# Kernel optimization log

Measured on AMD Instinct MI355X. Metric: run time of the kernel, lower is better.

Reference implementation:

```python
import jax, jax.numpy as jnp
import numpy as np

B, S, D, H, FF = 2, 2048, 1024, 16, 4096
HD = D // H
EPS = 1e-9


def setup_inputs() -> dict:
    key = jax.random.key(0)
    ks = jax.random.split(key, 16)
    sc = 0.02
    inp = {
        "x": jax.random.normal(ks[0], (B, S, D), jnp.float32),
        "y": jax.random.normal(ks[1], (B, S, D), jnp.float32),
        "decoder_mask": jnp.tril(jnp.ones((S, S), jnp.int32))[None, None],  # [1,1,S,S]
        # self-attention params (weights stored [in,out])
        "qkv_w": jax.random.normal(ks[2], (D, 3 * D), jnp.float32) * sc,
        "qkv_b": jnp.zeros((3 * D,), jnp.float32),
        "sa_fc_w": jax.random.normal(ks[3], (D, D), jnp.float32) * sc,
        "sa_fc_b": jnp.zeros((D,), jnp.float32),
        "g1": jnp.ones((D,), jnp.float32),
        "b1": jnp.zeros((D,), jnp.float32),
        # cross-attention params
        "kv_w": jax.random.normal(ks[4], (D, 2 * D), jnp.float32) * sc,
        "kv_b": jnp.zeros((2 * D,), jnp.float32),
        "q_w": jax.random.normal(ks[5], (D, D), jnp.float32) * sc,
        "q_b": jnp.zeros((D,), jnp.float32),
        "ca_fc_w": jax.random.normal(ks[6], (D, D), jnp.float32) * sc,
        "ca_fc_b": jnp.zeros((D,), jnp.float32),
        "g2": jnp.ones((D,), jnp.float32),
        "b2": jnp.zeros((D,), jnp.float32),
        # FFN params
        "ff1_w": jax.random.normal(ks[7], (D, FF), jnp.float32) * sc,
        "ff1_b": jnp.zeros((FF,), jnp.float32),
        "ff2_w": jax.random.normal(ks[8], (FF, D), jnp.float32) * sc,
        "ff2_b": jnp.zeros((D,), jnp.float32),
        "g3": jnp.ones((D,), jnp.float32),
        "b3": jnp.zeros((D,), jnp.float32),
    }
    return inp


def _layernorm(x, g, b):
    mean = jnp.mean(x, axis=-1, keepdims=True)
    var = jnp.mean((x - mean) ** 2, axis=-1, keepdims=True)
    return g * (x - mean) / jnp.sqrt(var + EPS) + b


def _sdpa(q, k, v, mask=None):
    # q,k,v: [B,H,S,hd]
    scores = jnp.einsum("bhqd,bhkd->bhqk", q, k) / jnp.sqrt(jnp.float32(q.shape[-1]))
    if mask is not None:
        scores = jnp.where(mask == 0, jnp.float32(-1e9), scores)
    attn = jax.nn.softmax(scores, axis=-1)
    return jnp.einsum("bhqk,bhkd->bhqd", attn, v)


def reference(x, y, decoder_mask, qkv_w, qkv_b, sa_fc_w, sa_fc_b, g1, b1,
              kv_w, kv_b, q_w, q_b, ca_fc_w, ca_fc_b, g2, b2,
              ff1_w, ff1_b, ff2_w, ff2_b, g3, b3):
    b, s, d = y.shape
    # --- masked self-attention on y ---
    qkv = (y @ qkv_w + qkv_b).reshape(b, s, H, 3 * HD).transpose(0, 2, 1, 3)
    q, k, v = jnp.split(qkv, 3, axis=-1)
    vals = _sdpa(q, k, v, decoder_mask).transpose(0, 2, 1, 3).reshape(b, s, d)
    sa = vals @ sa_fc_w + sa_fc_b
    y = _layernorm(sa + y, g1, b1)
    # --- cross-attention: kv from x, q from y ---
    kv = (x @ kv_w + kv_b).reshape(b, s, H, 2 * HD).transpose(0, 2, 1, 3)
    k2, v2 = jnp.split(kv, 2, axis=-1)
    q2 = (y @ q_w + q_b).reshape(b, s, H, HD).transpose(0, 2, 1, 3)
    vals2 = _sdpa(q2, k2, v2, None).transpose(0, 2, 1, 3).reshape(b, s, d)
    ca = vals2 @ ca_fc_w + ca_fc_b
    y = _layernorm(ca + y, g2, b2)
    # --- FFN ---
    h = jax.nn.relu(y @ ff1_w + ff1_b)
    ff = h @ ff2_w + ff2_b
    y = _layernorm(ff + y, g3, b3)
    return y
```

## Files before the change

### kernel.cpp

```cpp
#include <hip/hip_runtime.h>

typedef unsigned short u16;
typedef unsigned int u32;
typedef __attribute__((ext_vector_type(4))) float f32x4;
typedef __attribute__((ext_vector_type(8))) __bf16 bf16x8;
typedef __attribute__((ext_vector_type(2))) __bf16 bf16x2;
typedef __attribute__((ext_vector_type(4))) u16 u16x4;

#define NB 2
#define NS 2048
#define ND 1024
#define NH 16
#define NHD 64
#define NFF 4096
#define NBS (NB * NS)

typedef const __attribute__((address_space(1))) unsigned int as1_u32;
typedef __attribute__((address_space(3))) unsigned int as3_u32;

__device__ __forceinline__ void gl_lds16(const u16* g, u16* l) {
  __builtin_amdgcn_global_load_lds((as1_u32*)g, (as3_u32*)l, 16, 0, 0);
}

__device__ __forceinline__ u16 f2bf(float f) {
  union { float f; unsigned u; } v; v.f = f;
  unsigned r = (v.u + 0x7FFFu + ((v.u >> 16) & 1u)) >> 16;
  return (u16)r;
}

__device__ __forceinline__ float bf2f(u16 u) {
  union { u32 u; float f; } v; v.u = ((u32)u) << 16; return v.f;
}

__device__ __forceinline__ u32 pkbf(float a, float b) {
  bf16x2 v; v[0] = (__bf16)a; v[1] = (__bf16)b;
  union { bf16x2 v; u32 u; } c; c.v = v; return c.u;
}

__device__ __forceinline__ char* lswz(void* base, int row, int bcol) {
  return (char*)base + row * 128 + (bcol ^ ((row & 7) << 4));
}
__device__ __forceinline__ const char* lswz(const void* base, int row, int bcol) {
  return (const char*)base + row * 128 + (bcol ^ ((row & 7) << 4));
}

struct WSeg { const float* src; u16* dst; int N; int tile0; };
struct PrepArgs {
  const float* y; u16* yb;
  const float* x; u16* xb;
  WSeg s[7];
};

__global__ __launch_bounds__(256) void prep_all(PrepArgs pa) {
  const int bid = blockIdx.x;
  const int tid = threadIdx.x;
  if (bid < 8192) {
    const float* in = (bid < 4096) ? pa.y : pa.x;
    u16* out = (bid < 4096) ? pa.yb : pa.xb;
    int i = (bid & 4095) * 256 + tid;
    f32x4 v = *reinterpret_cast<const f32x4*>(&in[(size_t)i * 4]);
    u16x4 o;
#pragma unroll
    for (int j = 0; j < 4; ++j) o[j] = f2bf(v[j]);
    *reinterpret_cast<u16x4*>(&out[(size_t)i * 4]) = o;
    return;
  }
  __shared__ float t[32][33];
  const int wb = bid - 8192;
  int si = 0;
#pragma unroll
  for (int i = 1; i < 7; ++i) si += (wb >= pa.s[i].tile0) ? 1 : 0;
  const WSeg sg = pa.s[si];
  const int tt = wb - sg.tile0;
  const int tilesx = sg.N >> 5;
  const int n0 = (tt % tilesx) * 32, k0 = (tt / tilesx) * 32;
  const int K = (si == 6) ? NFF : ND;
  const int tx = tid & 31, ty = tid >> 5;
#pragma unroll
  for (int i = ty; i < 32; i += 8) t[i][tx] = sg.src[(size_t)(k0 + i) * sg.N + n0 + tx];
  __syncthreads();
#pragma unroll
  for (int i = ty; i < 32; i += 8)
    sg.dst[(size_t)(n0 + i) * K + k0 + tx] = f2bf(t[tx][i]);
}

template <int TM, int OUTF32, int RELU, int HM, int HA>
__global__ __launch_bounds__(256) void gemm_bt(const u16* __restrict__ A,
                                               const u16* __restrict__ BT,
                                               const float* __restrict__ bias,
                                               float* __restrict__ Cf,
                                               u16* __restrict__ Cb,
                                               u16* __restrict__ VTo,
                                               int M, int N, int K) {
  constexpr int MR = TM / 32;
  constexpr int ACH = TM / 64;
  __shared__ __align__(16) u16 lA[2][TM * 32];
  __shared__ __align__(16) u16 lB[2][128 * 32];
  const int tid = threadIdx.x;
  const int lane = tid & 63, wave = tid >> 6;
  const u32 gx = gridDim.x;
  const u32 nwg = gx * gridDim.y;
  const u32 flat = blockIdx.y * gx + blockIdx.x;
  const u32 swz = (flat & 7) * (nwg >> 3) + (flat >> 3);
  const int bm = (swz / gx) * TM, bn = (swz % gx) * 128;
  const int wr = (wave >> 1) * (MR * 16), wc = (wave & 1) * 64;
  const int r16 = lane & 15, kg = lane >> 4;

  f32x4 acc[MR][4] = {};

  auto stage = [&](int buf, int k0) {
#pragma unroll
    for (int c = 0; c < ACH; ++c) {
      int chunk = c * 256 + tid;
      int r = chunk >> 2, kc = (chunk & 3) * 8;
      gl_lds16(&A[(size_t)(bm + r) * K + k0 + kc], &lA[buf][(c * 256 + wave * 64) * 8]);
    }
#pragma unroll
    for (int c = 0; c < 2; ++c) {
      int chunk = c * 256 + tid;
      int r = chunk >> 2, kc = (chunk & 3) * 8;
      gl_lds16(&BT[(size_t)(bn + r) * K + k0 + kc], &lB[buf][(c * 256 + wave * 64) * 8]);
    }
  };

  stage(0, 0);
  __syncthreads();

  const int nk = K / 32;
  for (int i = 0; i < nk; ++i) {
    const int cur = i & 1;
    if (i + 1 < nk) stage(cur ^ 1, (i + 1) * 32);

    bf16x8 af[MR], bfr[4];
#pragma unroll
    for (int m = 0; m < MR; ++m)
      af[m] = *reinterpret_cast<const bf16x8*>(&lA[cur][(wr + m * 16 + r16) * 32 + kg * 8]);
#pragma unroll
    for (int n = 0; n < 4; ++n)
      bfr[n] = *reinterpret_cast<const bf16x8*>(&lB[cur][(wc + n * 16 + r16) * 32 + kg * 8]);
    __builtin_amdgcn_s_setprio(1);
#pragma unroll
    for (int m = 0; m < MR; ++m)
#pragma unroll
      for (int n = 0; n < 4; ++n)
        acc[m][n] = __builtin_amdgcn_mfma_f32_16x16x32_bf16(af[m], bfr[n], acc[m][n], 0, 0, 0);
    __builtin_amdgcn_s_setprio(0);

    __syncthreads();
  }

#pragma unroll
  for (int m = 0; m < MR; ++m) {
    int row = bm + wr + m * 16 + kg * 4;
#pragma unroll
    for (int n = 0; n < 4; ++n) {
      int col = bn + wc + n * 16 + r16;
      float bv = bias[col];
      u16x4 ob;
#pragma unroll
      for (int j = 0; j < 4; ++j) {
        float v = acc[m][n][j] + bv;
        if (RELU) v = fmaxf(v, 0.f);
        if (OUTF32)
          Cf[(size_t)(row + j) * N + col] = v;
        else {
          ob[j] = f2bf(v);
          Cb[(size_t)(row + j) * N + col] = ob[j];
        }
      }
      if (HM > 0) {
        int c0 = col % HM;
        if (c0 >= HA) {
          int hh = col / HM;
          int d = c0 - HA;
          int bb = row >> 11;
          int s = row & (NS - 1);
          *reinterpret_cast<u16x4*>(
              &VTo[(((size_t)(bb * NH + hh)) * NHD + d) * NS + s]) = ob;
        }
      }
    }
  }
}

#define C1F 0.180336880f
#define OPSZ ((size_t)32 * NS * NHD)

template <int CAUSAL>
__global__ __launch_bounds__(512) void attn10(const u16* __restrict__ Qp, int qstride,
                                              int qhm, const u16* __restrict__ Kp,
                                              int kstride, int khm, int kha,
                                              const u16* __restrict__ VT,
                                              u16* __restrict__ OP,
                                              float2* __restrict__ ML) {
  const int bid = blockIdx.x;
  const int split = blockIdx.y;
  const int xcd = bid & 7, j5 = bid >> 3;
  const int bh = xcd + 8 * (j5 >> 3);
  int qt = j5 & 7;
  if (CAUSAL) qt = 7 - qt;
  const int b = bh >> 4, h = bh & 15;
  const int tid = threadIdx.x, lane = tid & 63, wave = tid >> 6;
  const int r16 = lane & 15, kg = lane >> 4;
  const int q0w = qt * 256 + wave * 32;

  __shared__ __align__(16) char lK[2][64 * 128];
  __shared__ __align__(16) char lV[2][64 * 128];
  __shared__ __align__(16) char lP[8][16 * 128];
  char* lPw = &lP[wave][0];

  const u16* qb = Qp + (size_t)b * NS * qstride + h * qhm;
  const u16* kb = Kp + (size_t)b * NS * kstride + h * khm + kha;
  const u16* vb = VT + (size_t)bh * NHD * NS;

  const int srow = tid >> 3;
  const int sbcol = (tid & 7) * 16;
  const int scol = (tid & 7) * 8;

  bf16x8 qf[2][2];
#pragma unroll
  for (int qn = 0; qn < 2; ++qn)
#pragma unroll
    for (int ks = 0; ks < 2; ++ks) {
      bf16x8 v = *reinterpret_cast<const bf16x8*>(
          &qb[(size_t)(q0w + qn * 16 + r16) * qstride + ks * 32 + kg * 8]);
#pragma unroll
      for (int e = 0; e < 8; ++e) v[e] = (__bf16)((float)v[e] * C1F);
      qf[qn][ks] = v;
    }

  f32x4 o_acc[2][4] = {};
  float m_run[2] = {-1e30f, -1e30f}, l_lane[2] = {0.f, 0.f};

  const int ntb = CAUSAL ? (4 * qt + 4) : (NS / 64);
  const int wnt = CAUSAL ? (q0w / 64 + 1) : (NS / 64);
  const int halfb = (ntb + 1) >> 1;
  const int t0 = split ? halfb : 0;
  const int t1 = split ? ntb : halfb;

  uint4 kreg, vreg;
  auto ldregs = [&](int t) {
    const int kv0 = t * 64;
    kreg = *reinterpret_cast<const uint4*>(&kb[(size_t)(kv0 + srow) * kstride + scol]);
    vreg = *reinterpret_cast<const uint4*>(&vb[(size_t)srow * NS + kv0 + scol]);
  };
  auto wrlds = [&](int buf) {
    *reinterpret_cast<uint4*>(lswz(lK[buf], srow, sbcol)) = kreg;
    *reinterpret_cast<uint4*>(lswz(lV[buf], srow, sbcol)) = vreg;
  };

  ldregs(t0);
  wrlds(0);
  __syncthreads();

  for (int t = t0; t < t1; ++t) {
    const int cur = (t - t0) & 1;
    const bool more = (t + 1 < t1);
    if (more) ldregs(t + 1);

    if (t < wnt) {
      const int kv0 = t * 64;
      const char* lKc = lK[cur];
      const char* lVc = lV[cur];

      bf16x8 kf[8];
#pragma unroll
      for (int c = 0; c < 4; ++c)
#pragma unroll
        for (int ks = 0; ks < 2; ++ks)
          kf[c * 2 + ks] = *reinterpret_cast<const bf16x8*>(
              lswz(lKc, c * 16 + r16, ks * 64 + kg * 16));

      f32x4 s[2][4] = {};
#pragma unroll
      for (int c = 0; c < 4; ++c)
#pragma unroll
        for (int ks = 0; ks < 2; ++ks) {
          s[0][c] = __builtin_amdgcn_mfma_f32_16x16x32_bf16(kf[c * 2 + ks], qf[0][ks], s[0][c], 0, 0, 0);
          s[1][c] = __builtin_amdgcn_mfma_f32_16x16x32_bf16(kf[c * 2 + ks], qf[1][ks], s[1][c], 0, 0, 0);
        }

      bf16x8 vf[8];
#pragma unroll
      for (int cd = 0; cd < 4; ++cd)
#pragma unroll
        for (int ks = 0; ks < 2; ++ks)
          vf[cd * 2 + ks] = *reinterpret_cast<const bf16x8*>(
              lswz(lVc, cd * 16 + r16, ks * 64 + kg * 16));

#pragma unroll
      for (int qn = 0; qn < 2; ++qn) {
        if (CAUSAL && t == wnt - 1) {
          const int q = q0w + qn * 16 + r16;
#pragma unroll
          for (int c = 0; c < 4; ++c)
#pragma unroll
            for (int j = 0; j < 4; ++j)
              if (kv0 + c * 16 + kg * 4 + j > q) s[qn][c][j] = -1e31f;
        }
        float m0 = fmaxf(fmaxf(s[qn][0][0], s[qn][0][1]), fmaxf(s[qn][0][2], s[qn][0][3]));
        float m1 = fmaxf(fmaxf(s[qn][1][0], s[qn][1][1]), fmaxf(s[qn][1][2], s[qn][1][3]));
        float m2 = fmaxf(fmaxf(s[qn][2][0], s[qn][2][1]), fmaxf(s[qn][2][2], s[qn][2][3]));
        float m3 = fmaxf(fmaxf(s[qn][3][0], s[qn][3][1]), fmaxf(s[qn][3][2], s[qn][3][3]));
        float mxr = fmaxf(fmaxf(m0, m1), fmaxf(m2, m3));
        float mn = m_run[qn];
        if (!__all(mxr <= mn + 8.f)) {
          float mz = mxr;
          mz = fmaxf(mz, __shfl_xor(mz, 16));
          mz = fmaxf(mz, __shfl_xor(mz, 32));
          mn = fmaxf(m_run[qn], mz);
          const float cr = exp2f(m_run[qn] - mn);
          m_run[qn] = mn;
          l_lane[qn] *= cr;
          float crow[4];
#pragma unroll
          for (int j = 0; j < 4; ++j) crow[j] = __shfl(cr, kg * 4 + j);
#pragma unroll
          for (int cd = 0; cd < 4; ++cd)
#pragma unroll
            for (int j = 0; j < 4; ++j) o_acc[qn][cd][j] *= crow[j];
        }
        float su = 0.f;
#pragma unroll
        for (int c = 0; c < 4; ++c)
#pragma unroll
          for (int j = 0; j < 4; ++j) {
            float p = exp2f(s[qn][c][j] - mn);
            s[qn][c][j] = p;
            su += p;
          }
        l_lane[qn] += su;

#pragma unroll
        for (int c = 0; c < 4; ++c) {
          uint2 w2 = {pkbf(s[qn][c][0], s[qn][c][1]), pkbf(s[qn][c][2], s[qn][c][3])};
          *reinterpret_cast<uint2*>(lswz(lPw, r16, c * 32 + kg * 8)) = w2;
        }
        bf16x8 pf[2];
#pragma unroll
        for (int ks = 0; ks < 2; ++ks)
          pf[ks] = *reinterpret_cast<const bf16x8*>(lswz(lPw, r16, ks * 64 + kg * 16));
#pragma unroll
        for (int cd = 0; cd < 4; ++cd)
#pragma unroll
          for (int ks = 0; ks < 2; ++ks)
            o_acc[qn][cd] = __builtin_amdgcn_mfma_f32_16x16x32_bf16(
                pf[ks], vf[cd * 2 + ks], o_acc[qn][cd], 0, 0, 0);
      }
    }

    if (more) wrlds(cur ^ 1);
    __syncthreads();
  }

  u16* op = OP + split * OPSZ + (size_t)bh * NS * NHD;
#pragma unroll
  for (int qn = 0; qn < 2; ++qn) {
    float l = l_lane[qn];
    l += __shfl_xor(l, 16);
    l += __shfl_xor(l, 32);
#pragma unroll
    for (int cd = 0; cd < 4; ++cd) {
      int col = cd * 16 + r16;
#pragma unroll
      for (int j = 0; j < 4; ++j) {
        int row = q0w + qn * 16 + kg * 4 + j;
        op[(size_t)row * NHD + col] = f2bf(o_acc[qn][cd][j]);
      }
    }
    if (kg == 0)
      ML[(size_t)split * 32 * NS + (size_t)bh * NS + q0w + qn * 16 + r16] =
          make_float2(m_run[qn], l);
  }
}

template <int NSPL>
__global__ __launch_bounds__(256) void attn_comb(const u16* __restrict__ OP,
                                                 const float2* __restrict__ ML,
                                                 u16* __restrict__ AO) {
  int idx = blockIdx.x * 256 + threadIdx.x;
  int dg = (idx & 7) * 8;
  int q = (idx >> 3) & (NS - 1);
  int bh = idx >> 14;
  int b = bh >> 4, h = bh & 15;
  float2 ml[NSPL];
  float M = -1e30f;
#pragma unroll
  for (int s = 0; s < NSPL; ++s) {
    ml[s] = ML[((size_t)(s * 32 + bh)) * NS + q];
    M = fmaxf(M, ml[s].x);
  }
  float wgt[NSPL], wsum = 0.f;
#pragma unroll
  for (int s = 0; s < NSPL; ++s) {
    wgt[s] = exp2f(ml[s].x - M);
    wsum += ml[s].y * wgt[s];
  }
  float linv = 1.f / wsum;
  size_t src = ((size_t)bh * NS + q) * NHD + dg;
  float acc[8] = {};
#pragma unroll
  for (int s = 0; s < NSPL; ++s) {
    uint4 r = *reinterpret_cast<const uint4*>(&OP[s * OPSZ + src]);
    const u16* e = reinterpret_cast<const u16*>(&r);
#pragma unroll
    for (int j = 0; j < 8; ++j) acc[j] += bf2f(e[j]) * wgt[s];
  }
  u16 out[8];
#pragma unroll
  for (int j = 0; j < 8; ++j) out[j] = f2bf(acc[j] * linv);
  *reinterpret_cast<uint4*>(&AO[((size_t)b * NS + q) * ND + h * NHD + dg]) =
      *reinterpret_cast<uint4*>(out);
}

__global__ __launch_bounds__(256) void ln_kern(const float* __restrict__ a,
                                               const float* __restrict__ resid,
                                               const float* __restrict__ g,
                                               const float* __restrict__ bb,
                                               float* __restrict__ outf,
                                               u16* __restrict__ outb) {
  const int row = blockIdx.x;
  const int tid = threadIdx.x;
  const size_t off = (size_t)row * ND + tid * 4;
  f32x4 v = *reinterpret_cast<const f32x4*>(&a[off]);
  f32x4 r = *reinterpret_cast<const f32x4*>(&resid[off]);
#pragma unroll
  for (int j = 0; j < 4; ++j) v[j] += r[j];
  float s = v[0] + v[1] + v[2] + v[3];
  float s2 = v[0] * v[0] + v[1] * v[1] + v[2] * v[2] + v[3] * v[3];
#pragma unroll
  for (int m = 1; m < 64; m <<= 1) {
    s += __shfl_xor(s, m);
    s2 += __shfl_xor(s2, m);
  }
  __shared__ float ws1[4], ws2[4];
  int wave = tid >> 6, lane = tid & 63;
  if (lane == 0) { ws1[wave] = s; ws2[wave] = s2; }
  __syncthreads();
  s = ws1[0] + ws1[1] + ws1[2] + ws1[3];
  s2 = ws2[0] + ws2[1] + ws2[2] + ws2[3];
  float mean = s * (1.f / ND);
  float var = fmaxf(s2 * (1.f / ND) - mean * mean, 0.f);
  float rstd = rsqrtf(var + 1e-9f);
  f32x4 gg = *reinterpret_cast<const f32x4*>(&g[tid * 4]);
  f32x4 bv = *reinterpret_cast<const f32x4*>(&bb[tid * 4]);
  f32x4 o;
  u16x4 ob;
#pragma unroll
  for (int j = 0; j < 4; ++j) {
    o[j] = gg[j] * (v[j] - mean) * rstd + bv[j];
    ob[j] = f2bf(o[j]);
  }
  *reinterpret_cast<f32x4*>(&outf[off]) = o;
  *reinterpret_cast<u16x4*>(&outb[off]) = ob;
}

extern "C" void kernel_launch(void* const* d_in, const int* in_sizes, int n_in,
                              void* d_out, int out_size, void* d_ws, size_t ws_size,
                              hipStream_t stream) {
  const float* x = (const float*)d_in[0];
  const float* y = (const float*)d_in[1];
  const float* qkv_w = (const float*)d_in[3];
  const float* qkv_b = (const float*)d_in[4];
  const float* sa_fc_w = (const float*)d_in[5];
  const float* sa_fc_b = (const float*)d_in[6];
  const float* g1 = (const float*)d_in[7];
  const float* b1 = (const float*)d_in[8];
  const float* kv_w = (const float*)d_in[9];
  const float* kv_b = (const float*)d_in[10];
  const float* q_w = (const float*)d_in[11];
  const float* q_b = (const float*)d_in[12];
  const float* ca_fc_w = (const float*)d_in[13];
  const float* ca_fc_b = (const float*)d_in[14];
  const float* g2 = (const float*)d_in[15];
  const float* b2 = (const float*)d_in[16];
  const float* ff1_w = (const float*)d_in[17];
  const float* ff1_b = (const float*)d_in[18];
  const float* ff2_w = (const float*)d_in[19];
  const float* ff2_b = (const float*)d_in[20];
  const float* g3 = (const float*)d_in[21];
  const float* b3 = (const float*)d_in[22];

  if (ws_size < (120ull << 20)) return;

  char* w = (char*)d_ws;
  u16* Wqkv = (u16*)w;
  u16* Wsa  = Wqkv + 3145728;
  u16* Wkv  = Wsa + 1048576;
  u16* Wq   = Wkv + 2097152;
  u16* Wca  = Wq + 1048576;
  u16* Wff1 = Wca + 1048576;
  u16* Wff2 = Wff1 + 4194304;
  u16* ACT = (u16*)(w + (32ull << 20));
  u16* XB  = (u16*)(w + (40ull << 20));
  u16* Qb  = (u16*)(w + (48ull << 20));
  u16* VT  = (u16*)(w + (56ull << 20));
  u16* G   = (u16*)(w + (64ull << 20));
  float* Fa = (float*)(w + (88ull << 20));
  float* Fb = (float*)(w + (104ull << 20));
  u16* H   = XB;
  u16* AO  = G;
  u16* OPb = (u16*)Fa;
  float2* ML = (float2*)ACT;
  float* OUT = (float*)d_out;

  PrepArgs pa;
  pa.y = y; pa.yb = ACT; pa.x = x; pa.xb = XB;
  pa.s[0] = {qkv_w, Wqkv, 3 * ND, 0};
  pa.s[1] = {sa_fc_w, Wsa, ND, 3072};
  pa.s[2] = {kv_w, Wkv, 2 * ND, 4096};
  pa.s[3] = {q_w, Wq, ND, 6144};
  pa.s[4] = {ca_fc_w, Wca, ND, 7168};
  pa.s[5] = {ff1_w, Wff1, NFF, 8192};
  pa.s[6] = {ff2_w, Wff2, ND, 12288};
  prep_all<<<24576, 256, 0, stream>>>(pa);

  gemm_bt<128, 0, 0, 192, 128><<<dim3(3 * ND / 128, NBS / 128), 256, 0, stream>>>(
      ACT, Wqkv, qkv_b, nullptr, G, VT, NBS, 3 * ND, ND);
  attn10<1><<<dim3(256, 2), 512, 0, stream>>>(G, 3 * ND, 192, G, 3 * ND, 192, 64, VT, OPb, ML);
  attn_comb<2><<<2048, 256, 0, stream>>>(OPb, ML, AO);
  gemm_bt<64, 1, 0, 0, 0><<<dim3(ND / 128, NBS / 64), 256, 0, stream>>>(
      AO, Wsa, sa_fc_b, Fa, nullptr, nullptr, NBS, ND, ND);
  ln_kern<<<NBS, 256, 0, stream>>>(Fa, y, g1, b1, Fb, ACT);

  gemm_bt<128, 0, 0, 128, 64><<<dim3(2 * ND / 128, NBS / 128), 256, 0, stream>>>(
      XB, Wkv, kv_b, nullptr, G, VT, NBS, 2 * ND, ND);
  gemm_bt<64, 0, 0, 0, 0><<<dim3(ND / 128, NBS / 64), 256, 0, stream>>>(
      ACT, Wq, q_b, nullptr, Qb, nullptr, NBS, ND, ND);
  attn10<0><<<dim3(256, 2), 512, 0, stream>>>(Qb, ND, 64, G, 2 * ND, 128, 0, VT, OPb, ML);
  attn_comb<2><<<2048, 256, 0, stream>>>(OPb, ML, AO);
  gemm_bt<64, 1, 0, 0, 0><<<dim3(ND / 128, NBS / 64), 256, 0, stream>>>(
      AO, Wca, ca_fc_b, Fa, nullptr, nullptr, NBS, ND, ND);
  ln_kern<<<NBS, 256, 0, stream>>>(Fa, Fb, g2, b2, Fb, ACT);

  gemm_bt<128, 0, 1, 0, 0><<<dim3(NFF / 128, NBS / 128), 256, 0, stream>>>(
      ACT, Wff1, ff1_b, nullptr, H, nullptr, NBS, NFF, ND);
  gemm_bt<64, 1, 0, 0, 0><<<dim3(ND / 128, NBS / 64), 256, 0, stream>>>(
      H, Wff2, ff2_b, Fa, nullptr, nullptr, NBS, ND, NFF);
  ln_kern<<<NBS, 256, 0, stream>>>(Fa, Fb, g3, b3, OUT, ACT);
}
```

Before: 450.5 us.

## Balance causal self-attention with quota-based split-KV work scheduling per query tile

Replaces the uniform two-way split self-attention kernel with a scheduler that gives each 256-row query tile a number of KV splits proportional to its causal length (quota 1-4), producing 20 equal-ish work items per head. Blocks are mapped so each head's items land on one XCD, and a new combine kernel merges a variable number of partials per query row. This aims to remove load imbalance from the causal triangle, at the cost of more partial outputs to combine and constant-table lookups.

```diff
diff --git a/kernel.cpp b/kernel.cpp
--- a/kernel.cpp
+++ b/kernel.cpp
@@ -43,6 +43,11 @@
 __device__ __forceinline__ const char* lswz(const void* base, int row, int bcol) {
   return (const char*)base + row * 128 + (bcol ^ ((row & 7) << 4));
 }
+
+__device__ __constant__ int cQT[20]   = {7,7,7,7,6,6,6,6,5,5,5,4,4,4,3,3,2,2,1,0};
+__device__ __constant__ int cSUB[20]  = {0,1,2,3,0,1,2,3,0,1,2,0,1,2,0,1,0,1,0,0};
+__device__ __constant__ int cSLOTB[8] = {19,18,16,14,11,8,4,0};
+__device__ __constant__ int cQUOTA[8] = {1,1,2,2,3,3,4,4};
 
 struct WSeg { const float* src; u16* dst; int N; int tile0; };
 struct PrepArgs {
@@ -372,6 +377,230 @@
       ML[(size_t)split * 32 * NS + (size_t)bh * NS + q0w + qn * 16 + r16] =
           make_float2(m_run[qn], l);
   }
+}
+
+__global__ __launch_bounds__(512) void attn13(const u16* __restrict__ Kp, int kstride,
+                                              int khm, int kha, int qhm,
+                                              const u16* __restrict__ VT,
+                                              u16* __restrict__ OP,
+                                              float2* __restrict__ ML) {
+  const int bid = blockIdx.x;
+  const int xcd = bid & 7, j = bid >> 3;
+  const int bh = xcd + 8 * (j / 20);
+  const int si = j % 20;
+  const int qt = cQT[si], sub = cSUB[si];
+  const int b = bh >> 4, h = bh & 15;
+  const int tid = threadIdx.x, lane = tid & 63, wave = tid >> 6;
+  const int r16 = lane & 15, kg = lane >> 4;
+  const int q0w = qt * 256 + wave * 32;
+
+  __shared__ __align__(16) char lK[2][64 * 128];
+  __shared__ __align__(16) char lV[2][64 * 128];
+  __shared__ __align__(16) char lP[8][16 * 128];
+  char* lPw = &lP[wave][0];
+
+  const u16* qb = Kp + (size_t)b * NS * kstride + h * qhm;
+  const u16* kb = Kp + (size_t)b * NS * kstride + h * khm + kha;
+  const u16* vb = VT + (size_t)bh * NHD * NS;
+
+  const int srow = tid >> 3;
+  const int sbcol = (tid & 7) * 16;
+  const int scol = (tid & 7) * 8;
+
+  bf16x8 qf[2][2];
+#pragma unroll
+  for (int qn = 0; qn < 2; ++qn)
+#pragma unroll
+    for (int ks = 0; ks < 2; ++ks) {
+      bf16x8 v = *reinterpret_cast<const bf16x8*>(
+          &qb[(size_t)(q0w + qn * 16 + r16) * kstride + ks * 32 + kg * 8]);
+#pragma unroll
+      for (int e = 0; e < 8; ++e) v[e] = (__bf16)((float)v[e] * C1F);
+      qf[qn][ks] = v;
+    }
+
+  f32x4 o_acc[2][4] = {};
+  float m_run[2] = {-1e30f, -1e30f}, l_lane[2] = {0.f, 0.f};
+
+  const int ntb = 4 * qt + 4;
+  const int wnt = q0w / 64 + 1;
+  const int Q = cQUOTA[qt];
+  const int t0 = (sub * ntb) / Q;
+  const int t1 = ((sub + 1) * ntb) / Q;
+
+  uint4 kreg, vreg;
+  auto ldregs = [&](int t) {
+    const int kv0 = t * 64;
+    kreg = *reinterpret_cast<const uint4*>(&kb[(size_t)(kv0 + srow) * kstride + scol]);
+    vreg = *reinterpret_cast<const uint4*>(&vb[(size_t)srow * NS + kv0 + scol]);
+  };
+  auto wrlds = [&](int buf) {
+    *reinterpret_cast<uint4*>(lswz(lK[buf], srow, sbcol)) = kreg;
+    *reinterpret_cast<uint4*>(lswz(lV[buf], srow, sbcol)) = vreg;
+  };
+
+  ldregs(t0);
+  wrlds(0);
+  __syncthreads();
+
+  for (int t = t0; t < t1; ++t) {
+    const int cur = (t - t0) & 1;
+    const bool more = (t + 1 < t1);
+    if (more) ldregs(t + 1);
+
+    if (t < wnt) {
+      const int kv0 = t * 64;
+      const char* lKc = lK[cur];
+      const char* lVc = lV[cur];
+
+      bf16x8 kf[8];
+#pragma unroll
+      for (int c = 0; c < 4; ++c)
+#pragma unroll
+        for (int ks = 0; ks < 2; ++ks)
+          kf[c * 2 + ks] = *reinterpret_cast<const bf16x8*>(
+              lswz(lKc, c * 16 + r16, ks * 64 + kg * 16));
+
+      f32x4 s[2][4] = {};
+#pragma unroll
+      for (int c = 0; c < 4; ++c)
+#pragma unroll
+        for (int ks = 0; ks < 2; ++ks) {
+          s[0][c] = __builtin_amdgcn_mfma_f32_16x16x32_bf16(kf[c * 2 + ks], qf[0][ks], s[0][c], 0, 0, 0);
+          s[1][c] = __builtin_amdgcn_mfma_f32_16x16x32_bf16(kf[c * 2 + ks], qf[1][ks], s[1][c], 0, 0, 0);
+        }
+
+      bf16x8 vf[8];
+#pragma unroll
+      for (int cd = 0; cd < 4; ++cd)
+#pragma unroll
+        for (int ks = 0; ks < 2; ++ks)
+          vf[cd * 2 + ks] = *reinterpret_cast<const bf16x8*>(
+              lswz(lVc, cd * 16 + r16, ks * 64 + kg * 16));
+
+#pragma unroll
+      for (int qn = 0; qn < 2; ++qn) {
+        if (t == wnt - 1) {
+          const int q = q0w + qn * 16 + r16;
+#pragma unroll
+          for (int c = 0; c < 4; ++c)
+#pragma unroll
+            for (int j2 = 0; j2 < 4; ++j2)
+              if (kv0 + c * 16 + kg * 4 + j2 > q) s[qn][c][j2] = -1e31f;
+        }
+        float m0 = fmaxf(fmaxf(s[qn][0][0], s[qn][0][1]), fmaxf(s[qn][0][2], s[qn][0][3]));
+        float m1 = fmaxf(fmaxf(s[qn][1][0], s[qn][1][1]), fmaxf(s[qn][1][2], s[qn][1][3]));
+        float m2 = fmaxf(fmaxf(s[qn][2][0], s[qn][2][1]), fmaxf(s[qn][2][2], s[qn][2][3]));
+        float m3 = fmaxf(fmaxf(s[qn][3][0], s[qn][3][1]), fmaxf(s[qn][3][2], s[qn][3][3]));
+        float mxr = fmaxf(fmaxf(m0, m1), fmaxf(m2, m3));
+        float mn = m_run[qn];
+        if (!__all(mxr <= mn + 8.f)) {
+          float mz = mxr;
+          mz = fmaxf(mz, __shfl_xor(mz, 16));
+          mz = fmaxf(mz, __shfl_xor(mz, 32));
+          mn = fmaxf(m_run[qn], mz);
+          const float cr = exp2f(m_run[qn] - mn);
+          m_run[qn] = mn;
+          l_lane[qn] *= cr;
+          float crow[4];
+#pragma unroll
+          for (int j2 = 0; j2 < 4; ++j2) crow[j2] = __shfl(cr, kg * 4 + j2);
+#pragma unroll
+          for (int cd = 0; cd < 4; ++cd)
+#pragma unroll
+            for (int j2 = 0; j2 < 4; ++j2) o_acc[qn][cd][j2] *= crow[j2];
+        }
+        float su = 0.f;
+#pragma unroll
+        for (int c = 0; c < 4; ++c)
+#pragma unroll
+          for (int j2 = 0; j2 < 4; ++j2) {
+            float p = exp2f(s[qn][c][j2] - mn);
+            s[qn][c][j2] = p;
+            su += p;
+          }
+        l_lane[qn] += su;
+
+#pragma unroll
+        for (int c = 0; c < 4; ++c) {
+          uint2 w2 = {pkbf(s[qn][c][0], s[qn][c][1]), pkbf(s[qn][c][2], s[qn][c][3])};
+          *reinterpret_cast<uint2*>(lswz(lPw, r16, c * 32 + kg * 8)) = w2;
+        }
+        bf16x8 pf[2];
+#pragma unroll
+        for (int ks = 0; ks < 2; ++ks)
+          pf[ks] = *reinterpret_cast<const bf16x8*>(lswz(lPw, r16, ks * 64 + kg * 16));
+#pragma unroll
+        for (int cd = 0; cd < 4; ++cd)
+#pragma unroll
+          for (int ks = 0; ks < 2; ++ks)
+            o_acc[qn][cd] = __builtin_amdgcn_mfma_f32_16x16x32_bf16(
+                pf[ks], vf[cd * 2 + ks], o_acc[qn][cd], 0, 0, 0);
+      }
+    }
+
+    if (more) wrlds(cur ^ 1);
+    __syncthreads();
+  }
+
+  const int slot = bh * 20 + cSLOTB[qt] + sub;
+  u16* op = OP + (size_t)slot * (256 * 64);
+#pragma unroll
+  for (int qn = 0; qn < 2; ++qn) {
+    float l = l_lane[qn];
+    l += __shfl_xor(l, 16);
+    l += __shfl_xor(l, 32);
+#pragma unroll
+    for (int cd = 0; cd < 4; ++cd) {
+      int col = cd * 16 + r16;
+#pragma unroll
+      for (int j2 = 0; j2 < 4; ++j2) {
+        int rl = wave * 32 + qn * 16 + kg * 4 + j2;
+        op[(size_t)rl * NHD + col] = f2bf(o_acc[qn][cd][j2]);
+      }
+    }
+    if (kg == 0)
+      ML[(size_t)slot * 256 + wave * 32 + qn * 16 + r16] = make_float2(m_run[qn], l);
+  }
+}
+
+__global__ __launch_bounds__(256) void comb_self(const u16* __restrict__ OP,
+                                                 const float2* __restrict__ ML,
+                                                 u16* __restrict__ AO) {
+  int idx = blockIdx.x * 256 + threadIdx.x;
+  int dg = (idx & 7) * 8;
+  int q = (idx >> 3) & (NS - 1);
+  int bh = idx >> 14;
+  int b = bh >> 4, h = bh & 15;
+  int qt = q >> 8;
+  int Q = cQUOTA[qt];
+  int base = bh * 20 + cSLOTB[qt];
+  int qr = q & 255;
+  float M = -1e30f;
+  float2 ml[4];
+  for (int s = 0; s < Q; ++s) {
+    ml[s] = ML[(size_t)(base + s) * 256 + qr];
+    M = fmaxf(M, ml[s].x);
+  }
+  float wgt[4], wsum = 0.f;
+  for (int s = 0; s < Q; ++s) {
+    wgt[s] = exp2f(ml[s].x - M);
+    wsum += ml[s].y * wgt[s];
+  }
+  float linv = 1.f / wsum;
+  float acc[8] = {};
+  for (int s = 0; s < Q; ++s) {
+    uint4 r = *reinterpret_cast<const uint4*>(
+        &OP[(size_t)(base + s) * (256 * 64) + (size_t)qr * 64 + dg]);
+    const u16* e = reinterpret_cast<const u16*>(&r);
+#pragma unroll
+    for (int j = 0; j < 8; ++j) acc[j] += bf2f(e[j]) * wgt[s];
+  }
+  u16 out[8];
+#pragma unroll
+  for (int j = 0; j < 8; ++j) out[j] = f2bf(acc[j] * linv);
+  *reinterpret_cast<uint4*>(&AO[((size_t)b * NS + q) * ND + h * NHD + dg]) =
+      *reinterpret_cast<uint4*>(out);
 }
 
 template <int NSPL>
@@ -517,8 +746,8 @@
 
   gemm_bt<128, 0, 0, 192, 128><<<dim3(3 * ND / 128, NBS / 128), 256, 0, stream>>>(
       ACT, Wqkv, qkv_b, nullptr, G, VT, NBS, 3 * ND, ND);
-  attn10<1><<<dim3(256, 2), 512, 0, stream>>>(G, 3 * ND, 192, G, 3 * ND, 192, 64, VT, OPb, ML);
-  attn_comb<2><<<2048, 256, 0, stream>>>(OPb, ML, AO);
+  attn13<<<640, 512, 0, stream>>>(G, 3 * ND, 192, 64, 192, VT, OPb, ML);
+  comb_self<<<2048, 256, 0, stream>>>(OPb, ML, AO);
   gemm_bt<64, 1, 0, 0, 0><<<dim3(ND / 128, NBS / 64), 256, 0, stream>>>(
       AO, Wsa, sa_fc_b, Fa, nullptr, nullptr, NBS, ND, ND);
   ln_kern<<<NBS, 256, 0, stream>>>(Fa, y, g1, b1, Fb, ACT);
```

Result: slower. 465.3 us (+3.3%).
